# Optimization experiments

Hardware: AMD Instinct MI355X
Metric: run time of the kernel (lower is better)

## Reference

```python
import jax, jax.numpy as jnp
import numpy as np

B, L, D, H = 2, 1024, 1024, 16
Dh = D // H


def setup_inputs() -> dict:
    key = jax.random.key(0)
    ks = jax.random.split(key, 11)
    w_scale = 1.0 / np.sqrt(D).astype(np.float32)
    def w(k):
        return jax.random.normal(k, (D, D), dtype=jnp.float32) * w_scale
    def b(k):
        return jax.random.normal(k, (D,), dtype=jnp.float32) * 0.01
    return {
        "x": jax.random.normal(ks[0], (B, L, D), dtype=jnp.float32),
        "Wq": w(ks[1]), "bq": b(ks[2]),
        "Wk1": w(ks[3]), "bk1": b(ks[4]),
        "Wv": w(ks[5]), "bv": b(ks[6]),
        "Wk2": w(ks[7]), "bk2": b(ks[8]),
        "Wp": w(ks[9]), "bp": b(ks[10]),
    }


def reference(x, Wq, bq, Wk1, bk1, Wv, bv, Wk2, bk2, Wp, bp):
    Bx, Lx, Dx = x.shape
    lin = lambda t, W, b_: t @ W + b_
    # AR branch: kernelized accumulation of K^T V
    Q = lin(x, Wq, bq).reshape(Bx, Lx, H, Dh)      # (B,L,H,Dh)
    K = lin(x, Wk1, bk1).reshape(Bx, Lx, H, Dh)
    V = lin(x, Wv, bv).reshape(Bx, Lx, H, Dh)
    Wacc = jnp.cumsum(jnp.einsum('blhd,blhe->blhde', K, V), axis=1)  # (B,L,H,Dh,Dh)
    O1 = jnp.einsum('blhd,blhde->blhe', Q, Wacc)   # (B,L,H,Dh)
    # MA branch on one-step residuals
    V_raw = x.reshape(Bx, Lx, H, Dh)
    E = V_raw[:, 1:] - O1[:, :-1]                  # (B,L-1,H,Dh)
    z = lin(x[:, :-1], Wk2, bk2) / jnp.sqrt(jnp.float32(Dx))
    k2 = jax.nn.sigmoid(z * 0.02).reshape(Bx, Lx - 1, H, Dh)
    q2 = -jax.nn.leaky_relu(-Q[:, :-1] / jnp.sqrt(jnp.float32(Dh)), negative_slope=0.02)
    WE = jnp.cumsum(jnp.einsum('blhd,blhe->blhde', k2, E), axis=1)  # (B,L-1,H,Dh,Dh)
    O2 = jnp.einsum('blhd,blhde->blhe', q2, WE)
    O2 = jnp.concatenate([jnp.zeros_like(O2[:, :1]), O2], axis=1)   # (B,L,H,Dh)
    y = (O1 + O2).reshape(Bx, Lx, Dx)
    return lin(y, Wp, bp)
```

## Files before the change

kernel.cpp:

```cpp
#include <hip/hip_runtime.h>
#include <hip/hip_bf16.h>
#include <math.h>

#define Bsz 2
#define Lsz 1024
#define Dsz 1024
#define Hsz 16
#define Dh 64
#define Mtot (Bsz*Lsz)
#define NC (Lsz/64)
#define LPAD 72

typedef __bf16 bf16_t;
typedef bf16_t bf16x8 __attribute__((ext_vector_type(8)));
typedef bf16_t bf16x4 __attribute__((ext_vector_type(4)));
typedef float f32x4v __attribute__((ext_vector_type(4)));

__device__ __forceinline__ void gload16(const void* g, void* l) {
    __builtin_amdgcn_global_load_lds(
        (const __attribute__((address_space(1))) unsigned int*)g,
        (__attribute__((address_space(3))) unsigned int*)l, 16, 0, 0);
}

template<int MODE>
__global__ __launch_bounds__(256) void bgemm_kernel(
    const bf16_t* __restrict__ A, const bf16_t* __restrict__ Bt,
    const float* b0, const float* b1, const float* b2, const float* b3,
    bf16_t* Qo, bf16_t* q2o, bf16_t* Ko, bf16_t* Vo, bf16_t* k2o, float* Cout)
{
    __shared__ __align__(16) bf16_t As[4][4096];
    __shared__ __align__(16) bf16_t Bs[4][4096];
    const int tid  = threadIdx.x;
    const int lane = tid & 63;
    const int wid  = tid >> 6;

    const int lin = blockIdx.x;
    const int xcd = lin & 7;
    const int t0  = lin >> 3;
    int brow, bcolg;
    if (MODE == 0) {
        brow  = (xcd & 1) * 8 + (t0 & 7);
        bcolg = (xcd >> 1) * 8 + (t0 >> 3);
    } else {
        brow  = (xcd & 3) * 4 + (t0 & 3);
        bcolg = (xcd >> 2) * 4 + (t0 >> 2);
    }
    const int row0  = brow * 128;
    const int col0g = bcolg * 128;
    const int p    = col0g >> 10;
    const int col0 = col0g & 1023;
    const int wr = (wid >> 1) * 64;
    const int wc = (wid & 1) * 64;

    const int srow = tid >> 2;
    const int scol = tid & 3;
    const int ssw  = (srow & 3) ^ ((srow >> 2) & 3);
    const int scol_sw = scol ^ ssw;
    const bf16_t* gA0 = A  + (size_t)(row0 + srow)       * 1024 + scol_sw * 8;
    const bf16_t* gA1 = A  + (size_t)(row0 + srow + 64)  * 1024 + scol_sw * 8;
    const bf16_t* gB0 = Bt + (size_t)(col0g + srow)      * 1024 + scol_sw * 8;
    const bf16_t* gB1 = Bt + (size_t)(col0g + srow + 64) * 1024 + scol_sw * 8;

    const int laneRow = lane & 15;
    const int kblk = lane >> 4;
    const int swz = (kblk ^ (laneRow & 3) ^ ((laneRow >> 2) & 3)) & 3;
    const int aoff = (wr + laneRow) * 32 + swz * 8;
    const int boff = (wc + laneRow) * 32 + swz * 8;

    f32x4v acc[4][4];
    #pragma unroll
    for (int i = 0; i < 4; ++i)
        #pragma unroll
        for (int j = 0; j < 4; ++j)
            acc[i][j] = (f32x4v){0.f, 0.f, 0.f, 0.f};

    auto stage = [&](int buf) {
        gload16(gA0, &As[buf][tid * 8]);
        gload16(gA1, &As[buf][(tid + 256) * 8]);
        gload16(gB0, &Bs[buf][tid * 8]);
        gload16(gB1, &Bs[buf][(tid + 256) * 8]);
        gA0 += 32; gA1 += 32; gB0 += 32; gB1 += 32;
    };

    stage(0); stage(1); stage(2);
    asm volatile("s_waitcnt vmcnt(8)" ::: "memory");
    __builtin_amdgcn_s_barrier();

    for (int t = 0; t < 32; ++t) {
        const int cur = t & 3;
        bf16x8 af[4], bfr[4];
        #pragma unroll
        for (int f = 0; f < 4; ++f) {
            af[f]  = *reinterpret_cast<const bf16x8*>(&As[cur][aoff + f * 512]);
            bfr[f] = *reinterpret_cast<const bf16x8*>(&Bs[cur][boff + f * 512]);
        }
        if (t < 29) stage((t + 3) & 3);
        #pragma unroll
        for (int i = 0; i < 4; ++i)
            #pragma unroll
            for (int j = 0; j < 4; ++j)
                acc[i][j] = __builtin_amdgcn_mfma_f32_16x16x32_bf16(af[i], bfr[j], acc[i][j], 0, 0, 0);
        if (t < 29)      { asm volatile("s_waitcnt vmcnt(8)" ::: "memory"); }
        else if (t == 29){ asm volatile("s_waitcnt vmcnt(4)" ::: "memory"); }
        else if (t == 30){ asm volatile("s_waitcnt vmcnt(0)" ::: "memory"); }
        if (t < 31) __builtin_amdgcn_s_barrier();
    }

    const int crowb = row0 + wr + kblk * 4;
    const int ccolb = col0 + wc + laneRow;
    const float* bias = (MODE == 1) ? b0 : (p == 0) ? b0 : (p == 1) ? b1 : (p == 2) ? b2 : b3;
    float bv[4];
    #pragma unroll
    for (int j = 0; j < 4; ++j) bv[j] = bias[ccolb + j * 16];
    #pragma unroll
    for (int i = 0; i < 4; ++i)
        #pragma unroll
        for (int j = 0; j < 4; ++j)
            #pragma unroll
            for (int e = 0; e < 4; ++e) {
                const float val = acc[i][j][e] + bv[j];
                const size_t idx = (size_t)(crowb + i * 16 + e) * 1024 + ccolb + j * 16;
                if (MODE == 1) {
                    Cout[idx] = val;
                } else if (p == 0) {
                    Qo[idx]  = (bf16_t)val;
                    q2o[idx] = (bf16_t)((val >= 0.f ? 0.02f * val : val) * 0.125f);
                } else if (p == 1) {
                    Ko[idx] = (bf16_t)val;
                } else if (p == 2) {
                    Vo[idx] = (bf16_t)val;
                } else {
                    k2o[idx] = (bf16_t)(1.f / (1.f + __expf(-val * 0.000625f)));
                }
            }
}

__global__ __launch_bounds__(256) void prep_kernel(
    const float* __restrict__ x, bf16_t* __restrict__ xb,
    const float* __restrict__ W0, const float* __restrict__ W1,
    const float* __restrict__ W2, const float* __restrict__ W3,
    const float* __restrict__ W4, bf16_t* __restrict__ Wt)
{
    const int z = blockIdx.z;
    const int tid = threadIdx.x;
    if (z == 5) {
        const int lin = blockIdx.y * 16 + blockIdx.x;
        #pragma unroll
        for (int u = 0; u < 8; ++u) {
            const size_t s = (size_t)lin * 2048 + u * 256 + tid;
            float4 v = *reinterpret_cast<const float4*>(&x[s * 4]);
            bf16x4 o;
            o[0] = (bf16_t)v.x; o[1] = (bf16_t)v.y; o[2] = (bf16_t)v.z; o[3] = (bf16_t)v.w;
            *reinterpret_cast<bf16x4*>(&xb[s * 4]) = o;
        }
        return;
    }
    const float* W = (z == 0) ? W0 : (z == 1) ? W1 : (z == 2) ? W2 : (z == 3) ? W3 : W4;
    bf16_t* T = Wt + (size_t)z * 1048576;

    __shared__ float Ls[64][65];
    const int k0 = blockIdx.x * 64;
    const int n0 = blockIdx.y * 64;
    const int r  = tid >> 4;
    const int c4 = (tid & 15) * 4;
    #pragma unroll
    for (int i = 0; i < 4; ++i) {
        float4 v = *reinterpret_cast<const float4*>(&W[(size_t)(k0 + r + i * 16) * Dsz + n0 + c4]);
        Ls[r + i * 16][c4 + 0] = v.x;
        Ls[r + i * 16][c4 + 1] = v.y;
        Ls[r + i * 16][c4 + 2] = v.z;
        Ls[r + i * 16][c4 + 3] = v.w;
    }
    __syncthreads();
    #pragma unroll
    for (int i = 0; i < 4; ++i) {
        const int n = r + i * 16;
        bf16x4 o;
        o[0] = (bf16_t)Ls[c4 + 0][n];
        o[1] = (bf16_t)Ls[c4 + 1][n];
        o[2] = (bf16_t)Ls[c4 + 2][n];
        o[3] = (bf16_t)Ls[c4 + 3][n];
        *reinterpret_cast<bf16x4*>(&T[(size_t)(n0 + n) * Dsz + k0 + c4]) = o;
    }
}

__global__ __launch_bounds__(256) void chunk_intra_kernel(
    const bf16_t* __restrict__ Ap, const bf16_t* __restrict__ Kp,
    const bf16_t* __restrict__ Vp, bf16_t* __restrict__ Oi, bf16_t* __restrict__ dT)
{
    __shared__ __align__(16) bf16_t sQ[64 * LPAD];
    __shared__ __align__(16) bf16_t sK[64 * LPAD];
    __shared__ __align__(16) bf16_t sKt[64 * LPAD];
    __shared__ __align__(16) bf16_t sVt[64 * LPAD];
    __shared__ __align__(16) bf16_t sP[64 * LPAD];

    const int bid = blockIdx.x;
    const int c  = bid & (NC - 1);
    const int bh = bid >> 4;
    const int b = bh >> 4, h = bh & 15;
    const int tid = threadIdx.x;
    const size_t gbase = ((size_t)b * Lsz + (size_t)c * 64) * Dsz + h * Dh;

    #pragma unroll
    for (int cc = tid; cc < 512; cc += 256) {
        const int j = cc >> 3;
        const int d0 = (cc & 7) * 8;
        const size_t g = gbase + (size_t)j * 1024 + d0;
        bf16x8 qv = *reinterpret_cast<const bf16x8*>(&Ap[g]);
        bf16x8 kv = *reinterpret_cast<const bf16x8*>(&Kp[g]);
        bf16x8 vv = *reinterpret_cast<const bf16x8*>(&Vp[g]);
        *reinterpret_cast<bf16x8*>(&sQ[j * LPAD + d0]) = qv;
        *reinterpret_cast<bf16x8*>(&sK[j * LPAD + d0]) = kv;
        #pragma unroll
        for (int i = 0; i < 8; ++i) {
            sKt[(d0 + i) * LPAD + j] = kv[i];
            sVt[(d0 + i) * LPAD + j] = vv[i];
        }
    }
    __syncthreads();

    const int w = tid >> 6;
    const int lane = tid & 63;
    const int lr = lane & 15;
    const int kb = lane >> 4;
    const int m0 = w * 16;

    f32x4v accp[4];
    #pragma unroll
    for (int n = 0; n < 4; ++n) accp[n] = (f32x4v){0.f, 0.f, 0.f, 0.f};
    #pragma unroll
    for (int kk = 0; kk < 2; ++kk) {
        bf16x8 a = *reinterpret_cast<const bf16x8*>(&sQ[(m0 + lr) * LPAD + kk * 32 + kb * 8]);
        #pragma unroll
        for (int n = 0; n < 4; ++n) {
            bf16x8 bb = *reinterpret_cast<const bf16x8*>(&sK[(n * 16 + lr) * LPAD + kk * 32 + kb * 8]);
            accp[n] = __builtin_amdgcn_mfma_f32_16x16x32_bf16(a, bb, accp[n], 0, 0, 0);
        }
    }
    f32x4v acct[4];
    #pragma unroll
    for (int n = 0; n < 4; ++n) acct[n] = (f32x4v){0.f, 0.f, 0.f, 0.f};
    #pragma unroll
    for (int kk = 0; kk < 2; ++kk) {
        bf16x8 a = *reinterpret_cast<const bf16x8*>(&sVt[(m0 + lr) * LPAD + kk * 32 + kb * 8]);
        #pragma unroll
        for (int n = 0; n < 4; ++n) {
            bf16x8 bb = *reinterpret_cast<const bf16x8*>(&sKt[(n * 16 + lr) * LPAD + kk * 32 + kb * 8]);
            acct[n] = __builtin_amdgcn_mfma_f32_16x16x32_bf16(a, bb, acct[n], 0, 0, 0);
        }
    }

    const size_t tbase = (size_t)bid * 4096;
    #pragma unroll
    for (int n = 0; n < 4; ++n)
        #pragma unroll
        for (int e = 0; e < 4; ++e) {
            const int r = m0 + kb * 4 + e;
            const int col = n * 16 + lr;
            dT[tbase + (size_t)r * 64 + col] = (bf16_t)acct[n][e];
            float pv = (col <= r) ? accp[n][e] : 0.f;
            sP[r * LPAD + col] = (bf16_t)pv;
        }
    __syncthreads();

    f32x4v acco[4];
    #pragma unroll
    for (int n = 0; n < 4; ++n) acco[n] = (f32x4v){0.f, 0.f, 0.f, 0.f};
    #pragma unroll
    for (int kk = 0; kk < 2; ++kk) {
        bf16x8 a = *reinterpret_cast<const bf16x8*>(&sP[(m0 + lr) * LPAD + kk * 32 + kb * 8]);
        #pragma unroll
        for (int n = 0; n < 4; ++n) {
            bf16x8 bb = *reinterpret_cast<const bf16x8*>(&sVt[(n * 16 + lr) * LPAD + kk * 32 + kb * 8]);
            acco[n] = __builtin_amdgcn_mfma_f32_16x16x32_bf16(a, bb, acco[n], 0, 0, 0);
        }
    }
    #pragma unroll
    for (int n = 0; n < 4; ++n)
        #pragma unroll
        for (int e = 0; e < 4; ++e)
            Oi[gbase + (size_t)(m0 + kb * 4 + e) * 1024 + n * 16 + lr] = (bf16_t)acco[n][e];
}

template<int BR>
__global__ __launch_bounds__(256) void chunk_inter_kernel(
    const bf16_t* __restrict__ Ap, const bf16_t* __restrict__ dT,
    const bf16_t* __restrict__ Oi, const float* __restrict__ xin,
    const float* __restrict__ o1in, float* __restrict__ O1out,
    bf16_t* __restrict__ ebout)
{
    __shared__ __align__(16) bf16_t sA[64 * LPAD];
    __shared__ __align__(16) bf16_t sT[64 * LPAD];

    const int bid = blockIdx.x;
    const int c  = bid & (NC - 1);
    const int bh = bid >> 4;
    const int b = bh >> 4, h = bh & 15;
    const int tid = threadIdx.x;
    const size_t gbase = ((size_t)b * Lsz + (size_t)c * 64) * Dsz + h * Dh;

    #pragma unroll
    for (int cc = tid; cc < 512; cc += 256) {
        const int j = cc >> 3;
        const int d0 = (cc & 7) * 8;
        bf16x8 av = *reinterpret_cast<const bf16x8*>(&Ap[gbase + (size_t)j * 1024 + d0]);
        *reinterpret_cast<bf16x8*>(&sA[j * LPAD + d0]) = av;
    }
    {
        const bf16_t* tb = dT + (size_t)bh * NC * 4096 + tid * 16;
        float acc[16];
        #pragma unroll
        for (int k = 0; k < 16; ++k) acc[k] = 0.f;
        for (int cc = 0; cc < c; ++cc) {
            bf16x8 v0 = *reinterpret_cast<const bf16x8*>(&tb[(size_t)cc * 4096]);
            bf16x8 v1 = *reinterpret_cast<const bf16x8*>(&tb[(size_t)cc * 4096 + 8]);
            #pragma unroll
            for (int k = 0; k < 8; ++k) { acc[k] += (float)v0[k]; acc[8 + k] += (float)v1[k]; }
        }
        const int row = tid >> 2;
        const int c16 = (tid & 3) * 16;
        bf16x8 o0, o1v;
        #pragma unroll
        for (int k = 0; k < 8; ++k) { o0[k] = (bf16_t)acc[k]; o1v[k] = (bf16_t)acc[8 + k]; }
        *reinterpret_cast<bf16x8*>(&sT[row * LPAD + c16]) = o0;
        *reinterpret_cast<bf16x8*>(&sT[row * LPAD + c16 + 8]) = o1v;
    }
    __syncthreads();

    const int w = tid >> 6;
    const int lane = tid & 63;
    const int lr = lane & 15;
    const int kb = lane >> 4;
    const int m0 = w * 16;

    f32x4v acc[4];
    #pragma unroll
    for (int n = 0; n < 4; ++n) acc[n] = (f32x4v){0.f, 0.f, 0.f, 0.f};
    #pragma unroll
    for (int kk = 0; kk < 2; ++kk) {
        bf16x8 a = *reinterpret_cast<const bf16x8*>(&sA[(m0 + lr) * LPAD + kk * 32 + kb * 8]);
        #pragma unroll
        for (int n = 0; n < 4; ++n) {
            bf16x8 bb = *reinterpret_cast<const bf16x8*>(&sT[(n * 16 + lr) * LPAD + kk * 32 + kb * 8]);
            acc[n] = __builtin_amdgcn_mfma_f32_16x16x32_bf16(a, bb, acc[n], 0, 0, 0);
        }
    }

    #pragma unroll
    for (int n = 0; n < 4; ++n)
        #pragma unroll
        for (int e = 0; e < 4; ++e) {
            const int iLoc = m0 + kb * 4 + e;
            const int lglob = c * 64 + iLoc;
            const size_t idx = gbase + (size_t)iLoc * 1024 + n * 16 + lr;
            const float val = acc[n][e] + (float)Oi[idx];
            if (BR == 1) {
                O1out[idx] = val;
                float ev = 0.f;
                if (lglob < Lsz - 1) ev = xin[idx + 1024] - val;
                ebout[idx] = (bf16_t)ev;
            } else {
                if (lglob < Lsz - 1) ebout[idx + 1024] = (bf16_t)(o1in[idx + 1024] + val);
                if (lglob == 0)      ebout[idx] = (bf16_t)(o1in[idx]);
            }
        }
}

extern "C" void kernel_launch(void* const* d_in, const int* in_sizes, int n_in,
                              void* d_out, int out_size, void* d_ws, size_t ws_size,
                              hipStream_t stream) {
    const float* x   = (const float*)d_in[0];
    const float* Wq  = (const float*)d_in[1];
    const float* bq  = (const float*)d_in[2];
    const float* Wk1 = (const float*)d_in[3];
    const float* bk1 = (const float*)d_in[4];
    const float* Wv  = (const float*)d_in[5];
    const float* bv  = (const float*)d_in[6];
    const float* Wk2 = (const float*)d_in[7];
    const float* bk2 = (const float*)d_in[8];
    const float* Wp  = (const float*)d_in[9];
    const float* bp  = (const float*)d_in[10];
    float* out = (float*)d_out;
    float* ws  = (float*)d_ws;

    const size_t mat = (size_t)Mtot * Dsz;
    float*  O1  = ws;
    bf16_t* Oib = (bf16_t*)(ws + 2 * mat);
    bf16_t* dT  = (bf16_t*)(ws + 3 * mat);
    bf16_t* xb  = (bf16_t*)(ws + 4 * mat);
    bf16_t* Wt  = (bf16_t*)(ws + 5 * mat);
    float*  bb  = ws + 7 * mat + mat / 2;
    bf16_t* Qr  = (bf16_t*)(bb);
    bf16_t* q2  = (bf16_t*)(bb + mat / 2);
    bf16_t* Kb  = (bf16_t*)(bb + mat);
    bf16_t* Vb  = (bf16_t*)(bb + 3 * mat / 2);
    bf16_t* k2  = (bf16_t*)(bb + 2 * mat);
    bf16_t* Eb  = (bf16_t*)(bb + 5 * mat / 2);
    bf16_t* yb  = Qr;

    dim3 block(256);

    prep_kernel<<<dim3(16, 16, 6), block, 0, stream>>>(x, xb, Wq, Wk1, Wv, Wk2, Wp, Wt);

    bgemm_kernel<0><<<dim3(512), block, 0, stream>>>(
        xb, Wt, bq, bk1, bv, bk2, Qr, q2, Kb, Vb, k2, nullptr);

    chunk_intra_kernel<<<dim3(512), block, 0, stream>>>(Qr, Kb, Vb, Oib, dT);
    chunk_inter_kernel<1><<<dim3(512), block, 0, stream>>>(Qr, dT, Oib, x, nullptr, O1, Eb);
    chunk_intra_kernel<<<dim3(512), block, 0, stream>>>(q2, k2, Eb, Oib, dT);
    chunk_inter_kernel<2><<<dim3(512), block, 0, stream>>>(q2, dT, Oib, nullptr, O1, nullptr, yb);

    bgemm_kernel<1><<<dim3(128), block, 0, stream>>>(
        yb, Wt + 4 * 1048576, bp, nullptr, nullptr, nullptr,
        nullptr, nullptr, nullptr, nullptr, nullptr, out);
}
```

Before: 100.7 us.

## Fuse four chunk scan kernels into one cooperative kernel with grid syncs

Replaces the intra/inter chunk kernels for both branches with a single cooperative kernel that keeps per-chunk intra results (Oi, E, P) in registers and shared memory, using grid.sync between phases. This removes three kernel launches and the global round-trips of Oi and E, and interleaves independent MFMA chains. In exchange it adds two grid-wide barriers, requires all 512 blocks to be co-resident (launch_bounds 256,2 with larger shared memory), and uses separate dT buffers per branch.

```diff
diff --git a/kernel.cpp b/kernel.cpp
--- a/kernel.cpp
+++ b/kernel.cpp
@@ -1,6 +1,9 @@
 #include <hip/hip_runtime.h>
 #include <hip/hip_bf16.h>
+#include <hip/hip_cooperative_groups.h>
 #include <math.h>
+
+namespace cg = cooperative_groups;
 
 #define Bsz 2
 #define Lsz 1024
@@ -184,15 +187,22 @@
     }
 }
 
-__global__ __launch_bounds__(256) void chunk_intra_kernel(
-    const bf16_t* __restrict__ Ap, const bf16_t* __restrict__ Kp,
-    const bf16_t* __restrict__ Vp, bf16_t* __restrict__ Oi, bf16_t* __restrict__ dT)
+__global__ __launch_bounds__(256, 2) void coop_scan_kernel(
+    const bf16_t* __restrict__ Qr, const bf16_t* __restrict__ q2p,
+    const bf16_t* __restrict__ Kp, const bf16_t* __restrict__ Vp,
+    const bf16_t* __restrict__ k2p, const float* __restrict__ x,
+    float* __restrict__ O1g, bf16_t* __restrict__ dT1, bf16_t* __restrict__ dT2,
+    bf16_t* __restrict__ yb)
 {
-    __shared__ __align__(16) bf16_t sQ[64 * LPAD];
-    __shared__ __align__(16) bf16_t sK[64 * LPAD];
+    __shared__ __align__(16) bf16_t sQ [64 * LPAD];
+    __shared__ __align__(16) bf16_t sK [64 * LPAD];
     __shared__ __align__(16) bf16_t sKt[64 * LPAD];
     __shared__ __align__(16) bf16_t sVt[64 * LPAD];
-    __shared__ __align__(16) bf16_t sP[64 * LPAD];
+    __shared__ __align__(16) bf16_t sP [64 * LPAD];
+    __shared__ __align__(16) bf16_t sq2[64 * LPAD];
+    __shared__ __align__(16) bf16_t sT [64 * LPAD];
+
+    cg::grid_group grid = cg::this_grid();
 
     const int bid = blockIdx.x;
     const int c  = bid & (NC - 1);
@@ -201,55 +211,47 @@
     const int tid = threadIdx.x;
     const size_t gbase = ((size_t)b * Lsz + (size_t)c * 64) * Dsz + h * Dh;
 
-    #pragma unroll
-    for (int cc = tid; cc < 512; cc += 256) {
-        const int j = cc >> 3;
-        const int d0 = (cc & 7) * 8;
-        const size_t g = gbase + (size_t)j * 1024 + d0;
-        bf16x8 qv = *reinterpret_cast<const bf16x8*>(&Ap[g]);
-        bf16x8 kv = *reinterpret_cast<const bf16x8*>(&Kp[g]);
-        bf16x8 vv = *reinterpret_cast<const bf16x8*>(&Vp[g]);
-        *reinterpret_cast<bf16x8*>(&sQ[j * LPAD + d0]) = qv;
-        *reinterpret_cast<bf16x8*>(&sK[j * LPAD + d0]) = kv;
-        #pragma unroll
-        for (int i = 0; i < 8; ++i) {
-            sKt[(d0 + i) * LPAD + j] = kv[i];
-            sVt[(d0 + i) * LPAD + j] = vv[i];
-        }
-    }
-    __syncthreads();
-
     const int w = tid >> 6;
     const int lane = tid & 63;
     const int lr = lane & 15;
     const int kb = lane >> 4;
     const int m0 = w * 16;
 
-    f32x4v accp[4];
-    #pragma unroll
-    for (int n = 0; n < 4; ++n) accp[n] = (f32x4v){0.f, 0.f, 0.f, 0.f};
+    #pragma unroll
+    for (int it = 0; it < 2; ++it) {
+        const int cc = tid + it * 256;
+        const int j = cc >> 3;
+        const int d0 = (cc & 7) * 8;
+        const size_t g = gbase + (size_t)j * 1024 + d0;
+        bf16x8 qv = *reinterpret_cast<const bf16x8*>(&Qr[g]);
+        bf16x8 kv = *reinterpret_cast<const bf16x8*>(&Kp[g]);
+        bf16x8 vv = *reinterpret_cast<const bf16x8*>(&Vp[g]);
+        *reinterpret_cast<bf16x8*>(&sQ[j * LPAD + d0]) = qv;
+        *reinterpret_cast<bf16x8*>(&sK[j * LPAD + d0]) = kv;
+        #pragma unroll
+        for (int i = 0; i < 8; ++i) {
+            sKt[(d0 + i) * LPAD + j] = kv[i];
+            sVt[(d0 + i) * LPAD + j] = vv[i];
+        }
+    }
+    __syncthreads();
+
+    f32x4v accp[4], acct[4];
+    #pragma unroll
+    for (int n = 0; n < 4; ++n) { accp[n] = (f32x4v){0,0,0,0}; acct[n] = (f32x4v){0,0,0,0}; }
     #pragma unroll
     for (int kk = 0; kk < 2; ++kk) {
-        bf16x8 a = *reinterpret_cast<const bf16x8*>(&sQ[(m0 + lr) * LPAD + kk * 32 + kb * 8]);
+        const int c0 = kk * 32 + kb * 8;
+        bf16x8 aq = *reinterpret_cast<const bf16x8*>(&sQ [(m0 + lr) * LPAD + c0]);
+        bf16x8 av = *reinterpret_cast<const bf16x8*>(&sVt[(m0 + lr) * LPAD + c0]);
         #pragma unroll
         for (int n = 0; n < 4; ++n) {
-            bf16x8 bb = *reinterpret_cast<const bf16x8*>(&sK[(n * 16 + lr) * LPAD + kk * 32 + kb * 8]);
-            accp[n] = __builtin_amdgcn_mfma_f32_16x16x32_bf16(a, bb, accp[n], 0, 0, 0);
-        }
-    }
-    f32x4v acct[4];
-    #pragma unroll
-    for (int n = 0; n < 4; ++n) acct[n] = (f32x4v){0.f, 0.f, 0.f, 0.f};
-    #pragma unroll
-    for (int kk = 0; kk < 2; ++kk) {
-        bf16x8 a = *reinterpret_cast<const bf16x8*>(&sVt[(m0 + lr) * LPAD + kk * 32 + kb * 8]);
-        #pragma unroll
-        for (int n = 0; n < 4; ++n) {
-            bf16x8 bb = *reinterpret_cast<const bf16x8*>(&sKt[(n * 16 + lr) * LPAD + kk * 32 + kb * 8]);
-            acct[n] = __builtin_amdgcn_mfma_f32_16x16x32_bf16(a, bb, acct[n], 0, 0, 0);
-        }
-    }
-
+            bf16x8 bk = *reinterpret_cast<const bf16x8*>(&sK [(n * 16 + lr) * LPAD + c0]);
+            bf16x8 bt = *reinterpret_cast<const bf16x8*>(&sKt[(n * 16 + lr) * LPAD + c0]);
+            accp[n] = __builtin_amdgcn_mfma_f32_16x16x32_bf16(aq, bk, accp[n], 0, 0, 0);
+            acct[n] = __builtin_amdgcn_mfma_f32_16x16x32_bf16(av, bt, acct[n], 0, 0, 0);
+        }
+    }
     const size_t tbase = (size_t)bid * 4096;
     #pragma unroll
     for (int n = 0; n < 4; ++n)
@@ -257,57 +259,29 @@
         for (int e = 0; e < 4; ++e) {
             const int r = m0 + kb * 4 + e;
             const int col = n * 16 + lr;
-            dT[tbase + (size_t)r * 64 + col] = (bf16_t)acct[n][e];
-            float pv = (col <= r) ? accp[n][e] : 0.f;
-            sP[r * LPAD + col] = (bf16_t)pv;
-        }
-    __syncthreads();
-
-    f32x4v acco[4];
-    #pragma unroll
-    for (int n = 0; n < 4; ++n) acco[n] = (f32x4v){0.f, 0.f, 0.f, 0.f};
+            dT1[tbase + (size_t)r * 64 + col] = (bf16_t)acct[n][e];
+            sP[r * LPAD + col] = (bf16_t)((col <= r) ? accp[n][e] : 0.f);
+        }
+    __syncthreads();
+
+    f32x4v oi1[4];
+    #pragma unroll
+    for (int n = 0; n < 4; ++n) oi1[n] = (f32x4v){0,0,0,0};
     #pragma unroll
     for (int kk = 0; kk < 2; ++kk) {
-        bf16x8 a = *reinterpret_cast<const bf16x8*>(&sP[(m0 + lr) * LPAD + kk * 32 + kb * 8]);
+        const int c0 = kk * 32 + kb * 8;
+        bf16x8 ap = *reinterpret_cast<const bf16x8*>(&sP[(m0 + lr) * LPAD + c0]);
         #pragma unroll
         for (int n = 0; n < 4; ++n) {
-            bf16x8 bb = *reinterpret_cast<const bf16x8*>(&sVt[(n * 16 + lr) * LPAD + kk * 32 + kb * 8]);
-            acco[n] = __builtin_amdgcn_mfma_f32_16x16x32_bf16(a, bb, acco[n], 0, 0, 0);
-        }
-    }
-    #pragma unroll
-    for (int n = 0; n < 4; ++n)
-        #pragma unroll
-        for (int e = 0; e < 4; ++e)
-            Oi[gbase + (size_t)(m0 + kb * 4 + e) * 1024 + n * 16 + lr] = (bf16_t)acco[n][e];
-}
-
-template<int BR>
-__global__ __launch_bounds__(256) void chunk_inter_kernel(
-    const bf16_t* __restrict__ Ap, const bf16_t* __restrict__ dT,
-    const bf16_t* __restrict__ Oi, const float* __restrict__ xin,
-    const float* __restrict__ o1in, float* __restrict__ O1out,
-    bf16_t* __restrict__ ebout)
-{
-    __shared__ __align__(16) bf16_t sA[64 * LPAD];
-    __shared__ __align__(16) bf16_t sT[64 * LPAD];
-
-    const int bid = blockIdx.x;
-    const int c  = bid & (NC - 1);
-    const int bh = bid >> 4;
-    const int b = bh >> 4, h = bh & 15;
-    const int tid = threadIdx.x;
-    const size_t gbase = ((size_t)b * Lsz + (size_t)c * 64) * Dsz + h * Dh;
-
-    #pragma unroll
-    for (int cc = tid; cc < 512; cc += 256) {
-        const int j = cc >> 3;
-        const int d0 = (cc & 7) * 8;
-        bf16x8 av = *reinterpret_cast<const bf16x8*>(&Ap[gbase + (size_t)j * 1024 + d0]);
-        *reinterpret_cast<bf16x8*>(&sA[j * LPAD + d0]) = av;
-    }
+            bf16x8 bv = *reinterpret_cast<const bf16x8*>(&sVt[(n * 16 + lr) * LPAD + c0]);
+            oi1[n] = __builtin_amdgcn_mfma_f32_16x16x32_bf16(ap, bv, oi1[n], 0, 0, 0);
+        }
+    }
+
+    grid.sync();
+
     {
-        const bf16_t* tb = dT + (size_t)bh * NC * 4096 + tid * 16;
+        const bf16_t* tb = dT1 + (size_t)bh * NC * 4096 + tid * 16;
         float acc[16];
         #pragma unroll
         for (int k = 0; k < 16; ++k) acc[k] = 0.f;
@@ -325,44 +299,121 @@
         *reinterpret_cast<bf16x8*>(&sT[row * LPAD + c16]) = o0;
         *reinterpret_cast<bf16x8*>(&sT[row * LPAD + c16 + 8]) = o1v;
     }
-    __syncthreads();
-
-    const int w = tid >> 6;
-    const int lane = tid & 63;
-    const int lr = lane & 15;
-    const int kb = lane >> 4;
-    const int m0 = w * 16;
-
-    f32x4v acc[4];
-    #pragma unroll
-    for (int n = 0; n < 4; ++n) acc[n] = (f32x4v){0.f, 0.f, 0.f, 0.f};
+    #pragma unroll
+    for (int it = 0; it < 2; ++it) {
+        const int cc = tid + it * 256;
+        const int j = cc >> 3;
+        const int d0 = (cc & 7) * 8;
+        const size_t g = gbase + (size_t)j * 1024 + d0;
+        bf16x8 qv = *reinterpret_cast<const bf16x8*>(&q2p[g]);
+        bf16x8 kv = *reinterpret_cast<const bf16x8*>(&k2p[g]);
+        *reinterpret_cast<bf16x8*>(&sq2[j * LPAD + d0]) = qv;
+        *reinterpret_cast<bf16x8*>(&sK [j * LPAD + d0]) = kv;
+        #pragma unroll
+        for (int i = 0; i < 8; ++i)
+            sKt[(d0 + i) * LPAD + j] = kv[i];
+    }
+    __syncthreads();
+
+    f32x4v acci[4];
+    #pragma unroll
+    for (int n = 0; n < 4; ++n) { acci[n] = (f32x4v){0,0,0,0}; accp[n] = (f32x4v){0,0,0,0}; }
     #pragma unroll
     for (int kk = 0; kk < 2; ++kk) {
-        bf16x8 a = *reinterpret_cast<const bf16x8*>(&sA[(m0 + lr) * LPAD + kk * 32 + kb * 8]);
+        const int c0 = kk * 32 + kb * 8;
+        bf16x8 aq  = *reinterpret_cast<const bf16x8*>(&sQ [(m0 + lr) * LPAD + c0]);
+        bf16x8 aq2 = *reinterpret_cast<const bf16x8*>(&sq2[(m0 + lr) * LPAD + c0]);
         #pragma unroll
         for (int n = 0; n < 4; ++n) {
-            bf16x8 bb = *reinterpret_cast<const bf16x8*>(&sT[(n * 16 + lr) * LPAD + kk * 32 + kb * 8]);
-            acc[n] = __builtin_amdgcn_mfma_f32_16x16x32_bf16(a, bb, acc[n], 0, 0, 0);
-        }
-    }
-
+            bf16x8 bs = *reinterpret_cast<const bf16x8*>(&sT[(n * 16 + lr) * LPAD + c0]);
+            bf16x8 bk = *reinterpret_cast<const bf16x8*>(&sK[(n * 16 + lr) * LPAD + c0]);
+            acci[n] = __builtin_amdgcn_mfma_f32_16x16x32_bf16(aq,  bs, acci[n], 0, 0, 0);
+            accp[n] = __builtin_amdgcn_mfma_f32_16x16x32_bf16(aq2, bk, accp[n], 0, 0, 0);
+        }
+    }
     #pragma unroll
     for (int n = 0; n < 4; ++n)
         #pragma unroll
         for (int e = 0; e < 4; ++e) {
             const int iLoc = m0 + kb * 4 + e;
-            const int lglob = c * 64 + iLoc;
+            const int col = n * 16 + lr;
+            const int lg = c * 64 + iLoc;
+            const size_t idx = gbase + (size_t)iLoc * 1024 + col;
+            const float o1 = oi1[n][e] + acci[n][e];
+            O1g[idx] = o1;
+            const float ev = (lg < Lsz - 1) ? (x[idx + 1024] - o1) : 0.f;
+            sVt[col * LPAD + iLoc] = (bf16_t)ev;
+            sP[iLoc * LPAD + col] = (bf16_t)((col <= iLoc) ? accp[n][e] : 0.f);
+        }
+    __syncthreads();
+
+    f32x4v oi2[4];
+    #pragma unroll
+    for (int n = 0; n < 4; ++n) { oi2[n] = (f32x4v){0,0,0,0}; acct[n] = (f32x4v){0,0,0,0}; }
+    #pragma unroll
+    for (int kk = 0; kk < 2; ++kk) {
+        const int c0 = kk * 32 + kb * 8;
+        bf16x8 ae = *reinterpret_cast<const bf16x8*>(&sVt[(m0 + lr) * LPAD + c0]);
+        bf16x8 ap = *reinterpret_cast<const bf16x8*>(&sP [(m0 + lr) * LPAD + c0]);
+        #pragma unroll
+        for (int n = 0; n < 4; ++n) {
+            bf16x8 bt = *reinterpret_cast<const bf16x8*>(&sKt[(n * 16 + lr) * LPAD + c0]);
+            bf16x8 be = *reinterpret_cast<const bf16x8*>(&sVt[(n * 16 + lr) * LPAD + c0]);
+            acct[n] = __builtin_amdgcn_mfma_f32_16x16x32_bf16(ae, bt, acct[n], 0, 0, 0);
+            oi2[n]  = __builtin_amdgcn_mfma_f32_16x16x32_bf16(ap, be, oi2[n],  0, 0, 0);
+        }
+    }
+    #pragma unroll
+    for (int n = 0; n < 4; ++n)
+        #pragma unroll
+        for (int e = 0; e < 4; ++e)
+            dT2[tbase + (size_t)(m0 + kb * 4 + e) * 64 + n * 16 + lr] = (bf16_t)acct[n][e];
+
+    grid.sync();
+
+    {
+        const bf16_t* tb = dT2 + (size_t)bh * NC * 4096 + tid * 16;
+        float acc[16];
+        #pragma unroll
+        for (int k = 0; k < 16; ++k) acc[k] = 0.f;
+        for (int cc = 0; cc < c; ++cc) {
+            bf16x8 v0 = *reinterpret_cast<const bf16x8*>(&tb[(size_t)cc * 4096]);
+            bf16x8 v1 = *reinterpret_cast<const bf16x8*>(&tb[(size_t)cc * 4096 + 8]);
+            #pragma unroll
+            for (int k = 0; k < 8; ++k) { acc[k] += (float)v0[k]; acc[8 + k] += (float)v1[k]; }
+        }
+        const int row = tid >> 2;
+        const int c16 = (tid & 3) * 16;
+        bf16x8 o0, o1v;
+        #pragma unroll
+        for (int k = 0; k < 8; ++k) { o0[k] = (bf16_t)acc[k]; o1v[k] = (bf16_t)acc[8 + k]; }
+        *reinterpret_cast<bf16x8*>(&sT[row * LPAD + c16]) = o0;
+        *reinterpret_cast<bf16x8*>(&sT[row * LPAD + c16 + 8]) = o1v;
+    }
+    __syncthreads();
+
+    #pragma unroll
+    for (int n = 0; n < 4; ++n) acci[n] = (f32x4v){0,0,0,0};
+    #pragma unroll
+    for (int kk = 0; kk < 2; ++kk) {
+        const int c0 = kk * 32 + kb * 8;
+        bf16x8 aq2 = *reinterpret_cast<const bf16x8*>(&sq2[(m0 + lr) * LPAD + c0]);
+        #pragma unroll
+        for (int n = 0; n < 4; ++n) {
+            bf16x8 bs = *reinterpret_cast<const bf16x8*>(&sT[(n * 16 + lr) * LPAD + c0]);
+            acci[n] = __builtin_amdgcn_mfma_f32_16x16x32_bf16(aq2, bs, acci[n], 0, 0, 0);
+        }
+    }
+    #pragma unroll
+    for (int n = 0; n < 4; ++n)
+        #pragma unroll
+        for (int e = 0; e < 4; ++e) {
+            const int iLoc = m0 + kb * 4 + e;
+            const int lg = c * 64 + iLoc;
             const size_t idx = gbase + (size_t)iLoc * 1024 + n * 16 + lr;
-            const float val = acc[n][e] + (float)Oi[idx];
-            if (BR == 1) {
-                O1out[idx] = val;
-                float ev = 0.f;
-                if (lglob < Lsz - 1) ev = xin[idx + 1024] - val;
-                ebout[idx] = (bf16_t)ev;
-            } else {
-                if (lglob < Lsz - 1) ebout[idx + 1024] = (bf16_t)(o1in[idx + 1024] + val);
-                if (lglob == 0)      ebout[idx] = (bf16_t)(o1in[idx]);
-            }
+            const float o2 = oi2[n][e] + acci[n][e];
+            if (lg < Lsz - 1) yb[idx + 1024] = (bf16_t)(O1g[idx + 1024] + o2);
+            if (lg == 0)      yb[idx] = (bf16_t)(O1g[idx]);
         }
 }
 
@@ -385,8 +436,8 @@
 
     const size_t mat = (size_t)Mtot * Dsz;
     float*  O1  = ws;
-    bf16_t* Oib = (bf16_t*)(ws + 2 * mat);
-    bf16_t* dT  = (bf16_t*)(ws + 3 * mat);
+    bf16_t* dT1 = (bf16_t*)(ws + 2 * mat);
+    bf16_t* dT2 = (bf16_t*)(ws + 3 * mat);
     bf16_t* xb  = (bf16_t*)(ws + 4 * mat);
     bf16_t* Wt  = (bf16_t*)(ws + 5 * mat);
     float*  bb  = ws + 7 * mat + mat / 2;
@@ -395,8 +446,7 @@
     bf16_t* Kb  = (bf16_t*)(bb + mat);
     bf16_t* Vb  = (bf16_t*)(bb + 3 * mat / 2);
     bf16_t* k2  = (bf16_t*)(bb + 2 * mat);
-    bf16_t* Eb  = (bf16_t*)(bb + 5 * mat / 2);
-    bf16_t* yb  = Qr;
+    bf16_t* yb  = (bf16_t*)(bb + 5 * mat / 2);
 
     dim3 block(256);
 
@@ -405,10 +455,14 @@
     bgemm_kernel<0><<<dim3(512), block, 0, stream>>>(
         xb, Wt, bq, bk1, bv, bk2, Qr, q2, Kb, Vb, k2, nullptr);
 
-    chunk_intra_kernel<<<dim3(512), block, 0, stream>>>(Qr, Kb, Vb, Oib, dT);
-    chunk_inter_kernel<1><<<dim3(512), block, 0, stream>>>(Qr, dT, Oib, x, nullptr, O1, Eb);
-    chunk_intra_kernel<<<dim3(512), block, 0, stream>>>(q2, k2, Eb, Oib, dT);
-    chunk_inter_kernel<2><<<dim3(512), block, 0, stream>>>(q2, dT, Oib, nullptr, O1, nullptr, yb);
+    {
+        void* args[] = {
+            (void*)&Qr, (void*)&q2, (void*)&Kb, (void*)&Vb, (void*)&k2,
+            (void*)&x, (void*)&O1, (void*)&dT1, (void*)&dT2, (void*)&yb
+        };
+        hipLaunchCooperativeKernel((const void*)coop_scan_kernel,
+                                   dim3(512), dim3(256), args, 0, stream);
+    }
 
     bgemm_kernel<1><<<dim3(128), block, 0, stream>>>(
         yb, Wt + 4 * 1048576, bp, nullptr, nullptr, nullptr,
```

After: 197.3 us. 95.9% more time.
